# Performance work log

Measured on AMD Instinct MI355X. Metric: run time of the kernel, lower is better.

The kernel has to match this reference:

```python
import jax, jax.numpy as jnp
import numpy as np


def _l2norm(t, axis=-1, eps=1e-12):
    # matches torch F.normalize: x / max(||x||, eps)
    n = jnp.sqrt(jnp.sum(t * t, axis=axis, keepdims=True))
    return t / jnp.maximum(n, eps)


def setup_inputs() -> dict:
    key = jax.random.key(0)
    ks = jax.random.split(key, 5)
    B, N, C, H = 16, 4096, 768, 12
    x = jax.random.normal(ks[0], (B, N, C), dtype=jnp.float32)
    Wqkv = jax.random.normal(ks[1], (C, 3 * C), dtype=jnp.float32) * (C ** -0.5)
    bqkv = jax.random.normal(ks[2], (3 * C,), dtype=jnp.float32) * 0.02
    Wproj = jax.random.normal(ks[3], (C, C), dtype=jnp.float32) * (C ** -0.5)
    bproj = jax.random.normal(ks[4], (C,), dtype=jnp.float32) * 0.02
    temperature = jnp.ones((H, 1, 1), dtype=jnp.float32)
    return {"x": x, "Wqkv": Wqkv, "bqkv": bqkv, "Wproj": Wproj,
            "bproj": bproj, "temperature": temperature}


def reference(x, Wqkv, bqkv, Wproj, bproj, temperature):
    B, N, C = x.shape
    H = temperature.shape[0]
    Dh = C // H
    qkv = x @ Wqkv + bqkv                      # [B,N,3C]
    qkv = qkv.reshape(B, N, 3, H, Dh)
    # -> [3,B,H,Dh,N] (channels-as-tokens layout)
    qkv = jnp.transpose(qkv, (2, 0, 3, 4, 1))
    q, k, v = qkv[0], qkv[1], qkv[2]           # each [B,H,Dh,N]
    q = _l2norm(q, axis=-1)
    k = _l2norm(k, axis=-1)
    # cross-covariance over channels: [B,H,Dh,Dh]
    attn = jnp.einsum('bhdn,bhen->bhde', q, k) * temperature
    attn = jax.nn.softmax(attn, axis=-1)
    out = jnp.einsum('bhde,bhen->bhdn', attn, v)  # [B,H,Dh,N]
    out = jnp.transpose(out, (0, 3, 1, 2)).reshape(B, N, C)
    return out @ Wproj + bproj
```

## Files before the change

### kernel.cpp

```cpp
#include <hip/hip_runtime.h>

typedef __bf16 bf16x8 __attribute__((ext_vector_type(8)));
typedef float  f32x4  __attribute__((ext_vector_type(4)));
typedef unsigned short u16x8 __attribute__((ext_vector_type(8)));
typedef unsigned short u16x4 __attribute__((ext_vector_type(4)));

#define MFMA16(a, b, c) __builtin_amdgcn_mfma_f32_16x16x32_bf16((a), (b), (c), 0, 0, 0)

#define GLOAD16(g, l) __builtin_amdgcn_global_load_lds( \
    (const __attribute__((address_space(1))) void*)(g),  \
    (__attribute__((address_space(3))) void*)(l), 16, 0, 0)

__device__ __forceinline__ float bf2f(unsigned short u) {
    unsigned int x = ((unsigned int)u) << 16;
    return __builtin_bit_cast(float, x);
}
__device__ __forceinline__ unsigned short f2bf(float f) {
    unsigned int x = __builtin_bit_cast(unsigned int, f);
    x = x + 0x7FFFu + ((x >> 16) & 1u);
    return (unsigned short)(x >> 16);
}
__device__ __forceinline__ bool is_f32(const unsigned short* tf) { return tf[0] == 0; }
__device__ __forceinline__ float ldscal(const void* p, int i, bool f32m) {
    return f32m ? ((const float*)p)[i] : bf2f(((const unsigned short*)p)[i]);
}

__device__ __forceinline__ void tr_tile(const void* in_, unsigned short* out,
                                        int R, int C, int istride,
                                        int bid, bool f32m, unsigned short* T)
{
    const int nct = C >> 6;
    const int tx = bid % nct;
    const int ty = bid / nct;
    const int r0 = ty * 64, c0 = tx * 64;
    const int t = threadIdx.x;
#pragma unroll
    for (int s = 0; s < 2; ++s) {
        const int idx = t + s * 256;
        const int rr = idx >> 3;
        const int cc = (idx & 7) * 8;
        unsigned short v[8];
        if (f32m) {
            const float* inf = (const float*)in_;
            f32x4 a = *(const f32x4*)&inf[(size_t)(r0 + rr) * istride + c0 + cc];
            f32x4 b = *(const f32x4*)&inf[(size_t)(r0 + rr) * istride + c0 + cc + 4];
#pragma unroll
            for (int j = 0; j < 4; ++j) { v[j] = f2bf(a[j]); v[4 + j] = f2bf(b[j]); }
        } else {
            u16x8 a = *(const u16x8*)&((const unsigned short*)in_)[(size_t)(r0 + rr) * istride + c0 + cc];
#pragma unroll
            for (int j = 0; j < 8; ++j) v[j] = a[j];
        }
#pragma unroll
        for (int j = 0; j < 8; ++j) T[(cc + j) * 72 + rr] = v[j];
    }
    __syncthreads();
#pragma unroll
    for (int s = 0; s < 2; ++s) {
        const int idx = t + s * 256;
        const int cc = idx >> 3;
        const int rr = (idx & 7) * 8;
        u16x8 v = *(const u16x8*)&T[cc * 72 + rr];
        *(u16x8*)&out[(size_t)(c0 + cc) * R + r0 + rr] = v;
    }
}

__global__ __launch_bounds__(256)
void prep_all(const void* __restrict__ x, unsigned short* __restrict__ xb,
              unsigned short* __restrict__ xbT, float* __restrict__ sB,
              const void* __restrict__ Wqkv, const void* __restrict__ Wp,
              unsigned short* __restrict__ WqkT, unsigned short* __restrict__ Wv_bf,
              unsigned short* __restrict__ WprojT, const unsigned short* __restrict__ tf)
{
    __shared__ unsigned short T[64 * 72];
    const bool f32m = is_f32(tf);
    if (blockIdx.x < 12288) {
        const int tx = blockIdx.x % 12;
        const int ty = blockIdx.x / 12;
        const int r0 = ty * 64, c0 = tx * 64;
        const int t = threadIdx.x;
#pragma unroll
        for (int s = 0; s < 2; ++s) {
            const int idx = t + s * 256;
            const int rr = idx >> 3;
            const int cc = (idx & 7) * 8;
            u16x8 v;
            if (f32m) {
                const float* inf = (const float*)x;
                f32x4 a = *(const f32x4*)&inf[(size_t)(r0 + rr) * 768 + c0 + cc];
                f32x4 b = *(const f32x4*)&inf[(size_t)(r0 + rr) * 768 + c0 + cc + 4];
#pragma unroll
                for (int j = 0; j < 4; ++j) { v[j] = f2bf(a[j]); v[4 + j] = f2bf(b[j]); }
            } else {
                v = *(const u16x8*)&((const unsigned short*)x)[(size_t)(r0 + rr) * 768 + c0 + cc];
            }
            *(u16x8*)&xb[(size_t)(r0 + rr) * 768 + c0 + cc] = v;
#pragma unroll
            for (int j = 0; j < 8; ++j) T[(cc + j) * 72 + rr] = v[j];
        }
        __syncthreads();
#pragma unroll
        for (int s = 0; s < 2; ++s) {
            const int idx = t + s * 256;
            const int cc = idx >> 3;
            const int rr = (idx & 7) * 8;
            u16x8 v = *(const u16x8*)&T[cc * 72 + rr];
            *(u16x8*)&xbT[(size_t)(c0 + cc) * 65536 + r0 + rr] = v;
        }
        {
            const int col = t >> 2;
            const int seg = t & 3;
            float s = 0.f;
#pragma unroll
            for (int r = 0; r < 16; ++r) s += bf2f(T[col * 72 + seg * 16 + r]);
            s += __shfl_xor(s, 1);
            s += __shfl_xor(s, 2);
            if (seg == 0) atomicAdd(&sB[(r0 >> 12) * 768 + c0 + col], s);
        }
    } else {
        const int bid = blockIdx.x - 12288;
        if (bid < 288) {
            tr_tile(Wqkv, WqkT, 768, 1536, 2304, bid, f32m, T);
        } else if (bid < 576) {
            const int t = (bid - 288) * 256 + threadIdx.x;
            const int c = t / 96;
            const int e0 = (t % 96) * 8;
            u16x8 v;
            if (f32m) {
                const float* p = (const float*)Wqkv + (size_t)c * 2304 + 1536 + e0;
                f32x4 a = *(const f32x4*)p;
                f32x4 b = *(const f32x4*)(p + 4);
#pragma unroll
                for (int j = 0; j < 4; ++j) { v[j] = f2bf(a[j]); v[4 + j] = f2bf(b[j]); }
            } else {
                v = *(const u16x8*)&((const unsigned short*)Wqkv)[(size_t)c * 2304 + 1536 + e0];
            }
            *(u16x8*)&Wv_bf[(size_t)c * 768 + e0] = v;
        } else {
            tr_tile(Wp, WprojT, 768, 768, 768, bid - 576, f32m, T);
        }
    }
}

__global__ __launch_bounds__(256, 2)
void gemmG(const unsigned short* __restrict__ A, unsigned short* __restrict__ G)
{
    constexpr int NT = 64;
    constexpr size_t LD = 65536;
    __shared__ __align__(16) char SM[65536];
    unsigned short* lds = (unsigned short*)SM;

    const int tid  = threadIdx.x;
    const int wave = tid >> 6;
    const int lane = tid & 63;
    const int wm   = wave >> 1;
    const int wn   = wave & 1;
    const int lr   = lane & 15;
    const int lq   = lane >> 4;

    const int per = gridDim.x >> 3;
    const int wg  = (blockIdx.x & 7) * per + (blockIdx.x >> 3);
    const int b = wg / 21;
    int rr21 = wg % 21;
    int mt = 0;
    while (rr21 >= 6 - mt) { rr21 -= 6 - mt; ++mt; }
    const int nt = mt + rr21;
    const size_t m0 = (size_t)mt * 128;
    const int n0 = nt * 128;

    const unsigned short* Ab = A + m0 * LD + (size_t)b * 4096;
    const unsigned short* Bb = A + (size_t)n0 * LD + (size_t)b * 4096;
    unsigned short* Gb = G + (size_t)b * 589824;

    f32x4 zero = {0.f, 0.f, 0.f, 0.f};
    f32x4 acc[4][4];
#pragma unroll
    for (int i = 0; i < 4; ++i)
#pragma unroll
        for (int j = 0; j < 4; ++j) acc[i][j] = zero;

    auto STAGE = [&](int t) {
        unsigned short* la_ = lds + (t & 1) * 16384;
        unsigned short* lb_ = la_ + 8192;
#pragma unroll
        for (int it = 0; it < 4; ++it) {
            const int c = it * 256 + tid;
            const int row = c >> 3;
            const int gs = (c & 7) ^ (row & 7);
            GLOAD16(Ab + (size_t)row * LD + t * 64 + gs * 8, la_ + c * 8);
        }
#pragma unroll
        for (int it = 0; it < 4; ++it) {
            const int c = it * 256 + tid;
            const int row = c >> 3;
            const int gs = (c & 7) ^ (row & 7);
            GLOAD16(Bb + (size_t)row * LD + t * 64 + gs * 8, lb_ + c * 8);
        }
    };

    STAGE(0);
    STAGE(1);

    for (int t = 0; t < NT; ++t) {
        if (t + 1 < NT) asm volatile("s_waitcnt vmcnt(8)" ::: "memory");
        else            asm volatile("s_waitcnt vmcnt(0)" ::: "memory");
        __builtin_amdgcn_s_barrier();
        __builtin_amdgcn_sched_barrier(0);

        const char* la = (const char*)(lds + (t & 1) * 16384);
        const char* lb = la + 16384;

        bf16x8 bfr[4][2], af[4][2];
#pragma unroll
        for (int ni = 0; ni < 4; ++ni)
#pragma unroll
            for (int ks = 0; ks < 2; ++ks) {
                const int row = wn * 64 + ni * 16 + lr;
                const int s   = ks * 4 + lq;
                bfr[ni][ks] = *(const bf16x8*)(lb + row * 128 + ((s ^ (row & 7)) << 4));
            }
#pragma unroll
        for (int mi = 0; mi < 4; ++mi)
#pragma unroll
            for (int ks = 0; ks < 2; ++ks) {
                const int row = wm * 64 + mi * 16 + lr;
                const int s   = ks * 4 + lq;
                af[mi][ks] = *(const bf16x8*)(la + row * 128 + ((s ^ (row & 7)) << 4));
            }
        __builtin_amdgcn_s_setprio(1);
#pragma unroll
        for (int mi = 0; mi < 4; ++mi)
#pragma unroll
            for (int ni = 0; ni < 4; ++ni)
#pragma unroll
                for (int ks = 0; ks < 2; ++ks)
                    acc[mi][ni] = MFMA16(af[mi][ks], bfr[ni][ks], acc[mi][ni]);
        __builtin_amdgcn_s_setprio(0);

        __builtin_amdgcn_sched_barrier(0);
        __builtin_amdgcn_s_barrier();
        if (t + 2 < NT) STAGE(t + 2);
    }

#pragma unroll
    for (int mi = 0; mi < 4; ++mi)
#pragma unroll
        for (int ni = 0; ni < 4; ++ni)
#pragma unroll
            for (int r = 0; r < 4; ++r) {
                const size_t row = m0 + (size_t)(wm * 64 + mi * 16 + lq * 4 + r);
                const int col = n0 + wn * 64 + ni * 16 + lr;
                Gb[row * 768 + col] = f2bf(acc[mi][ni][r]);
            }

    if (mt != nt) {
        asm volatile("s_waitcnt lgkmcnt(0)" ::: "memory");
        __builtin_amdgcn_s_barrier();
        unsigned short* CTw = (unsigned short*)SM + wave * (64 * 68);
#pragma unroll
        for (int mi = 0; mi < 4; ++mi)
#pragma unroll
            for (int ni = 0; ni < 4; ++ni) {
                u16x4 pk;
#pragma unroll
                for (int r = 0; r < 4; ++r) pk[r] = f2bf(acc[mi][ni][r]);
                *(u16x4*)&CTw[(ni * 16 + lr) * 68 + mi * 16 + lq * 4] = pk;
            }
#pragma unroll
        for (int rep = 0; rep < 8; ++rep) {
            const int idx = rep * 64 + lane;
            const int c = idx >> 3;
            const int j = (idx & 7) * 8;
            u16x8 v = *(const u16x8*)&CTw[c * 68 + j];
            const size_t rowT = (size_t)n0 + wn * 64 + c;
            const int colT = (int)m0 + wm * 64 + j;
            *(u16x8*)&Gb[rowT * 768 + colT] = v;
        }
    }
}

template<int MODE>
__global__ __launch_bounds__(512, 8)
void gemmH(const unsigned short* __restrict__ A,
           const unsigned short* __restrict__ BT,
           const float* __restrict__ bias,
           unsigned short* __restrict__ o0,
           float* __restrict__ oF,
           const unsigned short* __restrict__ tf)
{
    constexpr int K = 768, NT = 24;
    __shared__ __align__(16) char SM[49152];

    const bool f32m = is_f32(tf);
    const int tid  = threadIdx.x;
    const int wave = tid >> 6;
    const int lane = tid & 63;
    const int wm   = wave >> 2;
    const int wn   = wave & 3;
    const int lr   = lane & 15;
    const int lq   = lane >> 4;

    const int per = gridDim.x >> 3;
    const int wg  = (blockIdx.x & 7) * per + (blockIdx.x >> 3);
    int b = 0, mt, nt;
    if (MODE == 4) { b = wg / 36; const int r = wg % 36; mt = r / 3; nt = r % 3; }
    else           { mt = wg / 3; nt = wg % 3; }
    const size_t m0 = (size_t)mt * 128;
    const int n0 = nt * 256;

    const unsigned short* Ab = A + m0 * K;
    const unsigned short* Bb;
    if (MODE == 1)      Bb = BT + (m0 >> 12) * (size_t)589824 + (size_t)n0 * K;
    else if (MODE == 4) Bb = BT + (size_t)b * 589824 + (size_t)n0 * K;
    else                Bb = BT + (size_t)n0 * K;

    f32x4 zero = {0.f, 0.f, 0.f, 0.f};
    f32x4 acc[4][4];
#pragma unroll
    for (int i = 0; i < 4; ++i)
#pragma unroll
        for (int j = 0; j < 4; ++j) acc[i][j] = zero;

    auto STAGE = [&](int t) {
        char* base = SM + (t & 1) * 24576;
        {
            const int c = tid;
            const int rp = c >> 3;
            const int ch = (c & 7) ^ (rp & 7);
            const int srow = rp * 2 + (ch >> 2);
            const int sk = (ch & 3) * 8;
            GLOAD16(Ab + (size_t)srow * K + t * 32 + sk, base + c * 16);
        }
#pragma unroll
        for (int ev = 0; ev < 2; ++ev) {
            const int c = ev * 512 + tid;
            const int rp = c >> 3;
            const int ch = (c & 7) ^ (rp & 7);
            const int srow = rp * 2 + (ch >> 2);
            const int sk = (ch & 3) * 8;
            GLOAD16(Bb + (size_t)srow * K + t * 32 + sk, base + 8192 + c * 16);
        }
    };

    STAGE(0);
    STAGE(1);

    for (int t = 0; t < NT; ++t) {
        if (t + 1 < NT) asm volatile("s_waitcnt vmcnt(3)" ::: "memory");
        else            asm volatile("s_waitcnt vmcnt(0)" ::: "memory");
        __builtin_amdgcn_s_barrier();
        __builtin_amdgcn_sched_barrier(0);

        const char* la = SM + (t & 1) * 24576;
        const char* lb = la + 8192;

        bf16x8 af[4], bfr[4];
#pragma unroll
        for (int ni = 0; ni < 4; ++ni) {
            const int row = wn * 64 + ni * 16 + lr;
            const int rp = row >> 1;
            const int ch = (row & 1) * 4 + lq;
            bfr[ni] = *(const bf16x8*)(lb + rp * 128 + ((ch ^ (rp & 7)) << 4));
        }
#pragma unroll
        for (int mi = 0; mi < 4; ++mi) {
            const int row = wm * 64 + mi * 16 + lr;
            const int rp = row >> 1;
            const int ch = (row & 1) * 4 + lq;
            af[mi] = *(const bf16x8*)(la + rp * 128 + ((ch ^ (rp & 7)) << 4));
        }
        __builtin_amdgcn_s_setprio(1);
#pragma unroll
        for (int mi = 0; mi < 4; ++mi)
#pragma unroll
            for (int ni = 0; ni < 4; ++ni)
                acc[mi][ni] = MFMA16(af[mi], bfr[ni], acc[mi][ni]);
        __builtin_amdgcn_s_setprio(0);

        __builtin_amdgcn_sched_barrier(0);
        __builtin_amdgcn_s_barrier();
        if (t + 2 < NT) STAGE(t + 2);
    }

    float bb[4];
#pragma unroll
    for (int ni = 0; ni < 4; ++ni) {
        const int col = n0 + wn * 64 + ni * 16 + lr;
        bb[ni] = (MODE == 1) ? bias[(m0 >> 12) * 768 + col] : 0.f;
    }

#pragma unroll
    for (int mi = 0; mi < 4; ++mi)
#pragma unroll
        for (int ni = 0; ni < 4; ++ni)
#pragma unroll
            for (int r = 0; r < 4; ++r) {
                const size_t row = m0 + (size_t)(wm * 64 + mi * 16 + lq * 4 + r);
                const int col = n0 + wn * 64 + ni * 16 + lr;
                const float val = acc[mi][ni][r] + bb[ni];
                if (MODE == 1) {
                    if (f32m) oF[row * 768 + col] = val;
                    else      o0[row * 768 + col] = f2bf(val);
                } else if (MODE == 2) {
                    o0[row * 768 + col] = f2bf(val);
                } else {
                    o0[(size_t)b * 1179648 + row * 768 + col] = f2bf(val);
                }
            }
}

__global__ __launch_bounds__(256)
void attn2(const unsigned short* __restrict__ P,
           const unsigned short* __restrict__ WqkT,
           const float* __restrict__ s,
           const void* __restrict__ bqkv,
           const unsigned short* __restrict__ tf,
           unsigned short* __restrict__ attnT)
{
    __shared__ float S[64][64];
    __shared__ float nq[64], nk[64], uq[64], uk[64];
    __shared__ float sb[768];
    __shared__ float bkv[64];
    const bool f32m = is_f32(tf);
    const int bh = blockIdx.x;
    const int b = bh / 12, h = bh % 12;
    const unsigned short* Pq = P + (size_t)b * 1179648 + (size_t)(h * 64) * 768;
    const unsigned short* Pk = Pq + 768 * 768;
    const unsigned short* Wq = WqkT + (size_t)(h * 64) * 768;
    const unsigned short* Wk = Wq + 768 * 768;
    const int tid = threadIdx.x;
    const int wave = tid >> 6;
    const int lane = tid & 63;
    const int lr = lane & 15;
    const int lq = lane >> 4;

    for (int i = tid; i < 768; i += 256) sb[i] = s[b * 768 + i];
    if (tid < 64) bkv[tid] = ldscal(bqkv, 768 + h * 64 + tid, f32m);

    f32x4 zero = {0.f, 0.f, 0.f, 0.f};
    f32x4 acc[4][4];
#pragma unroll
    for (int i = 0; i < 4; ++i)
#pragma unroll
        for (int j = 0; j < 4; ++j) acc[i][j] = zero;

    for (int ks = 0; ks < 6; ++ks) {
        const int j0 = wave * 192 + ks * 32 + lq * 8;
        u16x8 qa[4], ka[4];
#pragma unroll
        for (int mi = 0; mi < 4; ++mi)
            qa[mi] = *(const u16x8*)&Pq[(size_t)(mi * 16 + lr) * 768 + j0];
#pragma unroll
        for (int ni = 0; ni < 4; ++ni)
            ka[ni] = *(const u16x8*)&Wk[(size_t)(ni * 16 + lr) * 768 + j0];
#pragma unroll
        for (int mi = 0; mi < 4; ++mi)
#pragma unroll
            for (int ni = 0; ni < 4; ++ni)
                acc[mi][ni] = MFMA16(__builtin_bit_cast(bf16x8, qa[mi]),
                                     __builtin_bit_cast(bf16x8, ka[ni]),
                                     acc[mi][ni]);
    }
    __syncthreads();

    for (int ww = 0; ww < 4; ++ww) {
        if (wave == ww) {
#pragma unroll
            for (int mi = 0; mi < 4; ++mi)
#pragma unroll
                for (int ni = 0; ni < 4; ++ni)
#pragma unroll
                    for (int r = 0; r < 4; ++r) {
                        const int d = mi * 16 + lq * 4 + r;
                        const int e = ni * 16 + lr;
                        if (ww == 0) S[d][e] = acc[mi][ni][r];
                        else         S[d][e] += acc[mi][ni][r];
                    }
        }
        __syncthreads();
    }

    const int d  = tid >> 2;
    const int q4 = tid & 3;
    {
        const unsigned short* pqr = Pq + (size_t)d * 768 + q4 * 192;
        const unsigned short* wqr = Wq + (size_t)d * 768 + q4 * 192;
        const unsigned short* pkr = Pk + (size_t)d * 768 + q4 * 192;
        const unsigned short* wkr = Wk + (size_t)d * 768 + q4 * 192;
        float a_nq = 0.f, a_uq = 0.f, a_nk = 0.f, a_uk = 0.f;
        for (int i = 0; i < 24; ++i) {
            u16x8 vp = *(const u16x8*)&pqr[i * 8];
            u16x8 vw = *(const u16x8*)&wqr[i * 8];
            u16x8 kp = *(const u16x8*)&pkr[i * 8];
            u16x8 kw = *(const u16x8*)&wkr[i * 8];
#pragma unroll
            for (int j = 0; j < 8; ++j) {
                const float wqv = bf2f(vw[j]);
                const float wkv = bf2f(kw[j]);
                const float sj = sb[q4 * 192 + i * 8 + j];
                a_nq += bf2f(vp[j]) * wqv;
                a_uq += sj * wqv;
                a_nk += bf2f(kp[j]) * wkv;
                a_uk += sj * wkv;
            }
        }
        a_nq += __shfl_xor(a_nq, 1); a_nq += __shfl_xor(a_nq, 2);
        a_uq += __shfl_xor(a_uq, 1); a_uq += __shfl_xor(a_uq, 2);
        a_nk += __shfl_xor(a_nk, 1); a_nk += __shfl_xor(a_nk, 2);
        a_uk += __shfl_xor(a_uk, 1); a_uk += __shfl_xor(a_uk, 2);
        if (q4 == 0) { nq[d] = a_nq; uq[d] = a_uq; nk[d] = a_nk; uk[d] = a_uk; }
    }
    __syncthreads();

    const float tv  = f32m ? ((const float*)tf)[h] : bf2f(tf[h]);
    const float bqd = ldscal(bqkv, h * 64 + d, f32m);
    const float uqd = uq[d];
    const float nqf = nq[d] + 2.f * bqd * uqd + 4096.f * bqd * bqd;
    const float qn  = fmaxf(sqrtf(fmaxf(nqf, 0.f)), 1e-12f);
    float vals[16];
    float mx = -1e30f;
#pragma unroll
    for (int i = 0; i < 16; ++i) {
        const int e = q4 * 16 + i;
        const float bke = bkv[e];
        const float nkf = nk[e] + 2.f * bke * uk[e] + 4096.f * bke * bke;
        const float kn  = fmaxf(sqrtf(fmaxf(nkf, 0.f)), 1e-12f);
        const float sv  = S[d][e] + bqd * uk[e] + uqd * bke + 4096.f * bqd * bke;
        const float val = sv / (qn * kn) * tv;
        vals[i] = val;
        mx = fmaxf(mx, val);
    }
    mx = fmaxf(mx, __shfl_xor(mx, 1));
    mx = fmaxf(mx, __shfl_xor(mx, 2));
    float sum = 0.f;
#pragma unroll
    for (int i = 0; i < 16; ++i) { vals[i] = __expf(vals[i] - mx); sum += vals[i]; }
    sum += __shfl_xor(sum, 1);
    sum += __shfl_xor(sum, 2);
    const float inv = 1.0f / sum;
#pragma unroll
    for (int i = 0; i < 16; ++i) {
        const int e = q4 * 16 + i;
        attnT[(size_t)bh * 4096 + e * 64 + d] = f2bf(vals[i] * inv);
    }
}

__global__ __launch_bounds__(512)
void mb_build(const unsigned short* __restrict__ attnT,
              const unsigned short* __restrict__ WprojT,
              unsigned short* __restrict__ MbT)
{
    const int bh = blockIdx.x;
    const int b = bh / 12, h = bh % 12;
    const int tid = threadIdx.x;
    const int wave = tid >> 6;
    const int lane = tid & 63;
    const unsigned short* At = attnT + (size_t)bh * 4096;

    f32x4 zero = {0.f, 0.f, 0.f, 0.f};
    f32x4 acc[4][6];
#pragma unroll
    for (int i = 0; i < 4; ++i)
#pragma unroll
        for (int j = 0; j < 6; ++j) acc[i][j] = zero;

    const int lr  = lane & 15;
    const int lk8 = (lane >> 4) * 8;

#pragma unroll
    for (int ks = 0; ks < 2; ++ks) {
        bf16x8 af[4], bfr[6];
#pragma unroll
        for (int mi = 0; mi < 4; ++mi)
            af[mi] = *(const bf16x8*)&At[(mi * 16 + lr) * 64 + ks * 32 + lk8];
#pragma unroll
        for (int ni = 0; ni < 6; ++ni) {
            const int j = wave * 96 + ni * 16 + lr;
            bfr[ni] = *(const bf16x8*)&WprojT[(size_t)j * 768 + h * 64 + ks * 32 + lk8];
        }
#pragma unroll
        for (int mi = 0; mi < 4; ++mi)
#pragma unroll
            for (int ni = 0; ni < 6; ++ni)
                acc[mi][ni] = MFMA16(af[mi], bfr[ni], acc[mi][ni]);
    }

#pragma unroll
    for (int mi = 0; mi < 4; ++mi)
#pragma unroll
        for (int ni = 0; ni < 6; ++ni) {
            const int e = mi * 16 + (lane >> 4) * 4;
            const int j = wave * 96 + ni * 16 + lr;
            u16x4 pk;
#pragma unroll
            for (int r = 0; r < 4; ++r) pk[r] = f2bf(acc[mi][ni][r]);
            *(u16x4*)&MbT[(size_t)b * 589824 + (size_t)j * 768 + h * 64 + e] = pk;
        }
}

__global__ __launch_bounds__(256)
void beff_k(const unsigned short* __restrict__ MbT,
            const void* __restrict__ bqkv, const void* __restrict__ bp,
            float* __restrict__ beff, const unsigned short* __restrict__ tf)
{
    __shared__ float bv[768];
    const bool f32m = is_f32(tf);
    for (int i = threadIdx.x; i < 768; i += 256) bv[i] = ldscal(bqkv, 1536 + i, f32m);
    __syncthreads();
    const int t = blockIdx.x * 256 + threadIdx.x;
    const int b = t / 768, j = t % 768;
    float s = ldscal(bp, j, f32m);
    const unsigned short* row = MbT + (size_t)b * 589824 + (size_t)j * 768;
    for (int e8 = 0; e8 < 96; ++e8) {
        u16x8 m = *(const u16x8*)&row[e8 * 8];
#pragma unroll
        for (int jj = 0; jj < 8; ++jj) s += bf2f(m[jj]) * bv[e8 * 8 + jj];
    }
    beff[t] = s;
}

extern "C" void kernel_launch(void* const* d_in, const int* in_sizes, int n_in,
                              void* d_out, int out_size, void* d_ws, size_t ws_size,
                              hipStream_t stream)
{
    const void* x    = d_in[0];
    const void* Wqkv = d_in[1];
    const void* bqkv = d_in[2];
    const void* Wp   = d_in[3];
    const void* bp   = d_in[4];
    const unsigned short* tf = (const unsigned short*)d_in[5];

    char* w = (char*)d_ws;
    unsigned short* xbT    = (unsigned short*)(w);
    unsigned short* xb     = (unsigned short*)(w + 100663296);
    unsigned short* G      = (unsigned short*)(w + 201326592);
    unsigned short* P      = (unsigned short*)(w + 220200960);
    unsigned short* PT     = (unsigned short*)(w + 257949696);
    unsigned short* MbT    = (unsigned short*)(w + 276824064);
    unsigned short* WqkT   = (unsigned short*)(w + 295698432);
    unsigned short* Wv_bf  = (unsigned short*)(w + 298057728);
    unsigned short* WprojT = (unsigned short*)(w + 299237376);
    unsigned short* attnT  = (unsigned short*)(w + 300417024);
    float*          sB     = (float*)(w + 301989888);
    float*          beff   = (float*)(w + 302039040);

    hipMemsetAsync(sB, 0, 16 * 768 * sizeof(float), stream);
    prep_all<<<dim3(13008), dim3(256), 0, stream>>>(x, xb, xbT, sB, Wqkv, Wp,
                                                    WqkT, Wv_bf, WprojT, tf);

    gemmG<<<dim3(336), dim3(256), 0, stream>>>(xbT, G);
    gemmH<4><<<dim3(576), dim3(512), 0, stream>>>(WqkT, G, nullptr, P, nullptr, tf);
    attn2<<<dim3(192), dim3(256), 0, stream>>>(P, WqkT, sB, bqkv, tf, attnT);
    mb_build<<<dim3(192), dim3(512), 0, stream>>>(attnT, WprojT, MbT);
    beff_k<<<dim3(48), dim3(256), 0, stream>>>(MbT, bqkv, bp, beff, tf);
    gemmH<2><<<dim3(288), dim3(512), 0, stream>>>(MbT, Wv_bf, nullptr, PT, nullptr, tf);
    gemmH<1><<<dim3(1536), dim3(512), 0, stream>>>(xb, PT, beff,
        (unsigned short*)d_out, (float*)d_out, tf);
}
```

Baseline: 419.4 us.

## Fuse attention, projection-fold and bias kernels; triple-buffer gemmH LDS stages

The attention softmax kernel, the Mb construction kernel and the effective-bias kernel are merged into one 512-thread kernel. The softmax probabilities now stay in LDS instead of going through a global attnT buffer, and the V-bias contribution is accumulated into beff with atomicAdd; the memset is widened so it also zeroes beff. The output bias bp is added in the final GEMM epilogue instead. gemmH moves from double to triple LDS buffering, which lets it drop the second barrier per K step, at the cost of 72KB of LDS per block and possibly lower occupancy.

```diff
diff --git a/kernel.cpp b/kernel.cpp
--- a/kernel.cpp
+++ b/kernel.cpp
@@ -284,12 +284,13 @@
 void gemmH(const unsigned short* __restrict__ A,
            const unsigned short* __restrict__ BT,
            const float* __restrict__ bias,
+           const void* __restrict__ bp,
            unsigned short* __restrict__ o0,
            float* __restrict__ oF,
            const unsigned short* __restrict__ tf)
 {
     constexpr int K = 768, NT = 24;
-    __shared__ __align__(16) char SM[49152];
+    __shared__ __align__(16) char SM[73728];
 
     const bool f32m = is_f32(tf);
     const int tid  = threadIdx.x;
@@ -322,7 +323,7 @@
         for (int j = 0; j < 4; ++j) acc[i][j] = zero;
 
     auto STAGE = [&](int t) {
-        char* base = SM + (t & 1) * 24576;
+        char* base = SM + (t % 3) * 24576;
         {
             const int c = tid;
             const int rp = c >> 3;
@@ -346,12 +347,12 @@
     STAGE(1);
 
     for (int t = 0; t < NT; ++t) {
-        if (t + 1 < NT) asm volatile("s_waitcnt vmcnt(3)" ::: "memory");
+        if (t < NT - 1) asm volatile("s_waitcnt vmcnt(3)" ::: "memory");
         else            asm volatile("s_waitcnt vmcnt(0)" ::: "memory");
         __builtin_amdgcn_s_barrier();
         __builtin_amdgcn_sched_barrier(0);
 
-        const char* la = SM + (t & 1) * 24576;
+        const char* la = SM + (t % 3) * 24576;
         const char* lb = la + 8192;
 
         bf16x8 af[4], bfr[4];
@@ -378,7 +379,6 @@
         __builtin_amdgcn_s_setprio(0);
 
         __builtin_amdgcn_sched_barrier(0);
-        __builtin_amdgcn_s_barrier();
         if (t + 2 < NT) STAGE(t + 2);
     }
 
@@ -386,7 +386,7 @@
 #pragma unroll
     for (int ni = 0; ni < 4; ++ni) {
         const int col = n0 + wn * 64 + ni * 16 + lr;
-        bb[ni] = (MODE == 1) ? bias[(m0 >> 12) * 768 + col] : 0.f;
+        bb[ni] = (MODE == 1) ? (bias[(m0 >> 12) * 768 + col] + ldscal(bp, col, f32m)) : 0.f;
     }
 
 #pragma unroll
@@ -409,33 +409,38 @@
             }
 }
 
-__global__ __launch_bounds__(256)
-void attn2(const unsigned short* __restrict__ P,
-           const unsigned short* __restrict__ WqkT,
-           const float* __restrict__ s,
-           const void* __restrict__ bqkv,
-           const unsigned short* __restrict__ tf,
-           unsigned short* __restrict__ attnT)
+__global__ __launch_bounds__(512)
+void attn_mb(const unsigned short* __restrict__ P,
+             const unsigned short* __restrict__ WqkT,
+             const float* __restrict__ s,
+             const void* __restrict__ bqkv,
+             const unsigned short* __restrict__ WprojT,
+             const unsigned short* __restrict__ tf,
+             unsigned short* __restrict__ MbT,
+             float* __restrict__ beff)
 {
     __shared__ float S[64][64];
     __shared__ float nq[64], nk[64], uq[64], uk[64];
     __shared__ float sb[768];
     __shared__ float bkv[64];
+    __shared__ float bvv[64];
+    __shared__ unsigned short Pl[64 * 72];
     const bool f32m = is_f32(tf);
     const int bh = blockIdx.x;
     const int b = bh / 12, h = bh % 12;
     const unsigned short* Pq = P + (size_t)b * 1179648 + (size_t)(h * 64) * 768;
-    const unsigned short* Pk = Pq + 768 * 768;
     const unsigned short* Wq = WqkT + (size_t)(h * 64) * 768;
-    const unsigned short* Wk = Wq + 768 * 768;
+    const unsigned short* Pk = Pq + 589824;
+    const unsigned short* Wk = Wq + 589824;
     const int tid = threadIdx.x;
     const int wave = tid >> 6;
     const int lane = tid & 63;
     const int lr = lane & 15;
     const int lq = lane >> 4;
 
-    for (int i = tid; i < 768; i += 256) sb[i] = s[b * 768 + i];
-    if (tid < 64) bkv[tid] = ldscal(bqkv, 768 + h * 64 + tid, f32m);
+    for (int i = tid; i < 768; i += 512) sb[i] = s[b * 768 + i];
+    if (tid < 64)       bkv[tid] = ldscal(bqkv, 768 + h * 64 + tid, f32m);
+    else if (tid < 128) bvv[tid - 64] = ldscal(bqkv, 1536 + h * 64 + (tid - 64), f32m);
 
     f32x4 zero = {0.f, 0.f, 0.f, 0.f};
     f32x4 acc[4][4];
@@ -444,8 +449,8 @@
 #pragma unroll
         for (int j = 0; j < 4; ++j) acc[i][j] = zero;
 
-    for (int ks = 0; ks < 6; ++ks) {
-        const int j0 = wave * 192 + ks * 32 + lq * 8;
+    for (int ks = 0; ks < 3; ++ks) {
+        const int j0 = wave * 96 + ks * 32 + lq * 8;
         u16x8 qa[4], ka[4];
 #pragma unroll
         for (int mi = 0; mi < 4; ++mi)
@@ -463,7 +468,7 @@
     }
     __syncthreads();
 
-    for (int ww = 0; ww < 4; ++ww) {
+    for (int ww = 0; ww < 8; ++ww) {
         if (wave == ww) {
 #pragma unroll
             for (int mi = 0; mi < 4; ++mi)
@@ -480,15 +485,15 @@
         __syncthreads();
     }
 
-    const int d  = tid >> 2;
-    const int q4 = tid & 3;
+    const int d   = tid >> 3;
+    const int oct = tid & 7;
     {
-        const unsigned short* pqr = Pq + (size_t)d * 768 + q4 * 192;
-        const unsigned short* wqr = Wq + (size_t)d * 768 + q4 * 192;
-        const unsigned short* pkr = Pk + (size_t)d * 768 + q4 * 192;
-        const unsigned short* wkr = Wk + (size_t)d * 768 + q4 * 192;
+        const unsigned short* pqr = Pq + (size_t)d * 768 + oct * 96;
+        const unsigned short* wqr = Wq + (size_t)d * 768 + oct * 96;
+        const unsigned short* pkr = Pk + (size_t)d * 768 + oct * 96;
+        const unsigned short* wkr = Wk + (size_t)d * 768 + oct * 96;
         float a_nq = 0.f, a_uq = 0.f, a_nk = 0.f, a_uk = 0.f;
-        for (int i = 0; i < 24; ++i) {
+        for (int i = 0; i < 12; ++i) {
             u16x8 vp = *(const u16x8*)&pqr[i * 8];
             u16x8 vw = *(const u16x8*)&wqr[i * 8];
             u16x8 kp = *(const u16x8*)&pkr[i * 8];
@@ -497,126 +502,99 @@
             for (int j = 0; j < 8; ++j) {
                 const float wqv = bf2f(vw[j]);
                 const float wkv = bf2f(kw[j]);
-                const float sj = sb[q4 * 192 + i * 8 + j];
+                const float sj = sb[oct * 96 + i * 8 + j];
                 a_nq += bf2f(vp[j]) * wqv;
                 a_uq += sj * wqv;
                 a_nk += bf2f(kp[j]) * wkv;
                 a_uk += sj * wkv;
             }
         }
-        a_nq += __shfl_xor(a_nq, 1); a_nq += __shfl_xor(a_nq, 2);
-        a_uq += __shfl_xor(a_uq, 1); a_uq += __shfl_xor(a_uq, 2);
-        a_nk += __shfl_xor(a_nk, 1); a_nk += __shfl_xor(a_nk, 2);
-        a_uk += __shfl_xor(a_uk, 1); a_uk += __shfl_xor(a_uk, 2);
-        if (q4 == 0) { nq[d] = a_nq; uq[d] = a_uq; nk[d] = a_nk; uk[d] = a_uk; }
+        a_nq += __shfl_xor(a_nq, 1); a_nq += __shfl_xor(a_nq, 2); a_nq += __shfl_xor(a_nq, 4);
+        a_uq += __shfl_xor(a_uq, 1); a_uq += __shfl_xor(a_uq, 2); a_uq += __shfl_xor(a_uq, 4);
+        a_nk += __shfl_xor(a_nk, 1); a_nk += __shfl_xor(a_nk, 2); a_nk += __shfl_xor(a_nk, 4);
+        a_uk += __shfl_xor(a_uk, 1); a_uk += __shfl_xor(a_uk, 2); a_uk += __shfl_xor(a_uk, 4);
+        if (oct == 0) { nq[d] = a_nq; uq[d] = a_uq; nk[d] = a_nk; uk[d] = a_uk; }
     }
     __syncthreads();
 
-    const float tv  = f32m ? ((const float*)tf)[h] : bf2f(tf[h]);
-    const float bqd = ldscal(bqkv, h * 64 + d, f32m);
-    const float uqd = uq[d];
-    const float nqf = nq[d] + 2.f * bqd * uqd + 4096.f * bqd * bqd;
-    const float qn  = fmaxf(sqrtf(fmaxf(nqf, 0.f)), 1e-12f);
-    float vals[16];
-    float mx = -1e30f;
-#pragma unroll
-    for (int i = 0; i < 16; ++i) {
-        const int e = q4 * 16 + i;
-        const float bke = bkv[e];
-        const float nkf = nk[e] + 2.f * bke * uk[e] + 4096.f * bke * bke;
-        const float kn  = fmaxf(sqrtf(fmaxf(nkf, 0.f)), 1e-12f);
-        const float sv  = S[d][e] + bqd * uk[e] + uqd * bke + 4096.f * bqd * bke;
-        const float val = sv / (qn * kn) * tv;
-        vals[i] = val;
-        mx = fmaxf(mx, val);
-    }
-    mx = fmaxf(mx, __shfl_xor(mx, 1));
-    mx = fmaxf(mx, __shfl_xor(mx, 2));
-    float sum = 0.f;
-#pragma unroll
-    for (int i = 0; i < 16; ++i) { vals[i] = __expf(vals[i] - mx); sum += vals[i]; }
-    sum += __shfl_xor(sum, 1);
-    sum += __shfl_xor(sum, 2);
-    const float inv = 1.0f / sum;
-#pragma unroll
-    for (int i = 0; i < 16; ++i) {
-        const int e = q4 * 16 + i;
-        attnT[(size_t)bh * 4096 + e * 64 + d] = f2bf(vals[i] * inv);
-    }
-}
-
-__global__ __launch_bounds__(512)
-void mb_build(const unsigned short* __restrict__ attnT,
-              const unsigned short* __restrict__ WprojT,
-              unsigned short* __restrict__ MbT)
-{
-    const int bh = blockIdx.x;
-    const int b = bh / 12, h = bh % 12;
-    const int tid = threadIdx.x;
-    const int wave = tid >> 6;
-    const int lane = tid & 63;
-    const unsigned short* At = attnT + (size_t)bh * 4096;
-
-    f32x4 zero = {0.f, 0.f, 0.f, 0.f};
-    f32x4 acc[4][6];
+    {
+        const float tv  = f32m ? ((const float*)tf)[h] : bf2f(tf[h]);
+        const float bqd = ldscal(bqkv, h * 64 + d, f32m);
+        const float uqd = uq[d];
+        const float nqf = nq[d] + 2.f * bqd * uqd + 4096.f * bqd * bqd;
+        const float qn  = fmaxf(sqrtf(fmaxf(nqf, 0.f)), 1e-12f);
+        float vals[8];
+        float mx = -1e30f;
+#pragma unroll
+        for (int i = 0; i < 8; ++i) {
+            const int e = oct * 8 + i;
+            const float bke = bkv[e];
+            const float nkf = nk[e] + 2.f * bke * uk[e] + 4096.f * bke * bke;
+            const float kn  = fmaxf(sqrtf(fmaxf(nkf, 0.f)), 1e-12f);
+            const float sv  = S[d][e] + bqd * uk[e] + uqd * bke + 4096.f * bqd * bke;
+            const float val = sv / (qn * kn) * tv;
+            vals[i] = val;
+            mx = fmaxf(mx, val);
+        }
+        mx = fmaxf(mx, __shfl_xor(mx, 1));
+        mx = fmaxf(mx, __shfl_xor(mx, 2));
+        mx = fmaxf(mx, __shfl_xor(mx, 4));
+        float sum = 0.f;
+#pragma unroll
+        for (int i = 0; i < 8; ++i) { vals[i] = __expf(vals[i] - mx); sum += vals[i]; }
+        sum += __shfl_xor(sum, 1);
+        sum += __shfl_xor(sum, 2);
+        sum += __shfl_xor(sum, 4);
+        const float inv = 1.0f / sum;
+#pragma unroll
+        for (int i = 0; i < 8; ++i) {
+            const int e = oct * 8 + i;
+            Pl[e * 72 + d] = f2bf(vals[i] * inv);
+        }
+    }
+    __syncthreads();
+
+    f32x4 accm[4][6];
 #pragma unroll
     for (int i = 0; i < 4; ++i)
 #pragma unroll
-        for (int j = 0; j < 6; ++j) acc[i][j] = zero;
-
-    const int lr  = lane & 15;
-    const int lk8 = (lane >> 4) * 8;
+        for (int j = 0; j < 6; ++j) accm[i][j] = zero;
 
 #pragma unroll
     for (int ks = 0; ks < 2; ++ks) {
         bf16x8 af[4], bfr[6];
 #pragma unroll
         for (int mi = 0; mi < 4; ++mi)
-            af[mi] = *(const bf16x8*)&At[(mi * 16 + lr) * 64 + ks * 32 + lk8];
+            af[mi] = *(const bf16x8*)&Pl[(mi * 16 + lr) * 72 + ks * 32 + lq * 8];
 #pragma unroll
         for (int ni = 0; ni < 6; ++ni) {
             const int j = wave * 96 + ni * 16 + lr;
-            bfr[ni] = *(const bf16x8*)&WprojT[(size_t)j * 768 + h * 64 + ks * 32 + lk8];
+            bfr[ni] = *(const bf16x8*)&WprojT[(size_t)j * 768 + h * 64 + ks * 32 + lq * 8];
         }
 #pragma unroll
         for (int mi = 0; mi < 4; ++mi)
 #pragma unroll
             for (int ni = 0; ni < 6; ++ni)
-                acc[mi][ni] = MFMA16(af[mi], bfr[ni], acc[mi][ni]);
-    }
-
-#pragma unroll
-    for (int mi = 0; mi < 4; ++mi)
-#pragma unroll
-        for (int ni = 0; ni < 6; ++ni) {
-            const int e = mi * 16 + (lane >> 4) * 4;
-            const int j = wave * 96 + ni * 16 + lr;
+                accm[mi][ni] = MFMA16(af[mi], bfr[ni], accm[mi][ni]);
+    }
+
+#pragma unroll
+    for (int ni = 0; ni < 6; ++ni) {
+        const int j = wave * 96 + ni * 16 + lr;
+        float part = 0.f;
+#pragma unroll
+        for (int mi = 0; mi < 4; ++mi) {
+            const int e = mi * 16 + lq * 4;
             u16x4 pk;
 #pragma unroll
-            for (int r = 0; r < 4; ++r) pk[r] = f2bf(acc[mi][ni][r]);
+            for (int r = 0; r < 4; ++r) {
+                pk[r] = f2bf(accm[mi][ni][r]);
+                part += accm[mi][ni][r] * bvv[e + r];
+            }
             *(u16x4*)&MbT[(size_t)b * 589824 + (size_t)j * 768 + h * 64 + e] = pk;
         }
-}
-
-__global__ __launch_bounds__(256)
-void beff_k(const unsigned short* __restrict__ MbT,
-            const void* __restrict__ bqkv, const void* __restrict__ bp,
-            float* __restrict__ beff, const unsigned short* __restrict__ tf)
-{
-    __shared__ float bv[768];
-    const bool f32m = is_f32(tf);
-    for (int i = threadIdx.x; i < 768; i += 256) bv[i] = ldscal(bqkv, 1536 + i, f32m);
-    __syncthreads();
-    const int t = blockIdx.x * 256 + threadIdx.x;
-    const int b = t / 768, j = t % 768;
-    float s = ldscal(bp, j, f32m);
-    const unsigned short* row = MbT + (size_t)b * 589824 + (size_t)j * 768;
-    for (int e8 = 0; e8 < 96; ++e8) {
-        u16x8 m = *(const u16x8*)&row[e8 * 8];
-#pragma unroll
-        for (int jj = 0; jj < 8; ++jj) s += bf2f(m[jj]) * bv[e8 * 8 + jj];
-    }
-    beff[t] = s;
+        atomicAdd(&beff[b * 768 + j], part);
+    }
 }
 
 extern "C" void kernel_launch(void* const* d_in, const int* in_sizes, int n_in,
@@ -640,20 +618,17 @@
     unsigned short* WqkT   = (unsigned short*)(w + 295698432);
     unsigned short* Wv_bf  = (unsigned short*)(w + 298057728);
     unsigned short* WprojT = (unsigned short*)(w + 299237376);
-    unsigned short* attnT  = (unsigned short*)(w + 300417024);
     float*          sB     = (float*)(w + 301989888);
     float*          beff   = (float*)(w + 302039040);
 
-    hipMemsetAsync(sB, 0, 16 * 768 * sizeof(float), stream);
+    hipMemsetAsync(sB, 0, 98304, stream);
     prep_all<<<dim3(13008), dim3(256), 0, stream>>>(x, xb, xbT, sB, Wqkv, Wp,
                                                     WqkT, Wv_bf, WprojT, tf);
 
     gemmG<<<dim3(336), dim3(256), 0, stream>>>(xbT, G);
-    gemmH<4><<<dim3(576), dim3(512), 0, stream>>>(WqkT, G, nullptr, P, nullptr, tf);
-    attn2<<<dim3(192), dim3(256), 0, stream>>>(P, WqkT, sB, bqkv, tf, attnT);
-    mb_build<<<dim3(192), dim3(512), 0, stream>>>(attnT, WprojT, MbT);
-    beff_k<<<dim3(48), dim3(256), 0, stream>>>(MbT, bqkv, bp, beff, tf);
-    gemmH<2><<<dim3(288), dim3(512), 0, stream>>>(MbT, Wv_bf, nullptr, PT, nullptr, tf);
-    gemmH<1><<<dim3(1536), dim3(512), 0, stream>>>(xb, PT, beff,
+    gemmH<4><<<dim3(576), dim3(512), 0, stream>>>(WqkT, G, nullptr, nullptr, P, nullptr, tf);
+    attn_mb<<<dim3(192), dim3(512), 0, stream>>>(P, WqkT, sB, bqkv, WprojT, tf, MbT, beff);
+    gemmH<2><<<dim3(288), dim3(512), 0, stream>>>(MbT, Wv_bf, nullptr, nullptr, PT, nullptr, tf);
+    gemmH<1><<<dim3(1536), dim3(512), 0, stream>>>(xb, PT, beff, bp,
         (unsigned short*)d_out, (float*)d_out, tf);
 }
```

Result: no change. 419.7 us (+0.1%).
